# Kernel tuning notes

Hardware: AMD Instinct MI355X
Metric: run time of the kernel (lower is better)

Reference implementation:

```python
import jax, jax.numpy as jnp
import numpy as np

K = 1024   # num_embeddings
E = 64     # embedding_dim
T = 1024   # time
B = 64     # batch
BETA = 0.25  # commitment_cost


def setup_inputs() -> dict:
    key = jax.random.key(0)
    k1, k2 = jax.random.split(key)
    inputs = jax.random.normal(k1, (E, T, B), dtype=jnp.float32)
    # torch init: uniform(-1/num_embeddings, 1/num_embeddings)
    codebook = jax.random.uniform(k2, (K, E), dtype=jnp.float32,
                                  minval=-1.0 / K, maxval=1.0 / K)
    return {"inputs": inputs, "codebook": codebook}


def reference(inputs, codebook):
    # inputs: [E, T, B]; torch does permute(1,2,0) -> [T, B, E]
    x = jnp.transpose(inputs, (1, 2, 0))            # [T, B, E]
    flat = x.reshape(-1, E)                          # [N, E], N = T*B
    d = (jnp.sum(flat * flat, axis=1, keepdims=True)
         + jnp.sum(codebook * codebook, axis=1)
         - 2.0 * (flat @ codebook.T))
    idx = jnp.argmin(d, axis=1)                      # [N]
    # one-hot @ codebook == gather (same math, efficient form)
    q = codebook[idx].reshape(T, B, E)               # [T, B, E]

    e_latent_loss = jnp.mean((jax.lax.stop_gradient(q) - x) ** 2)
    q_latent_loss = jnp.mean((q - jax.lax.stop_gradient(x)) ** 2)
    vq_loss = q_latent_loss + BETA * e_latent_loss

    # straight-through estimator
    q_st = x + jax.lax.stop_gradient(q - x)

    # perplexity from code-usage histogram (mean of one-hots)
    N = flat.shape[0]
    counts = jnp.zeros((K,), jnp.float32).at[idx].add(1.0)
    avg_probs = counts / N
    perplexity = jnp.exp(-jnp.sum(avg_probs * jnp.log(avg_probs + 1e-10)))

    quantized = jnp.transpose(q_st, (2, 0, 1))       # back to [E, T, B]
    return vq_loss, quantized, perplexity
```

## Files before the change

kernel.cpp:

```cpp
#include <hip/hip_runtime.h>


#define KC 1024
#define ED 64
#define NR 65536
#define NE (NR * ED)
#define GAP1 6e-6f

typedef __attribute__((ext_vector_type(8))) short short8;
typedef __attribute__((ext_vector_type(4))) float f32x4;

__device__ __forceinline__ unsigned short bf16rne(float f) {
    unsigned u = __builtin_bit_cast(unsigned, f);
    return (unsigned short)((u + 0x7fffu + ((u >> 16) & 1u)) >> 16);
}
__device__ __forceinline__ float bf16tof(unsigned short h) {
    return __builtin_bit_cast(float, (unsigned)h << 16);
}

__global__ __launch_bounds__(256) void k_pack(const float* __restrict__ cb,
        short8* __restrict__ cbt, unsigned* __restrict__ counts,
        unsigned* __restrict__ flagcnt) {
    const int u = blockIdx.x * 256 + threadIdx.x;
    if (u < 1024) counts[u] = 0u;
    if (u == 1024) *flagcnt = 0u;
    if (u >= 64 * 5 * 64) return;
    const int t = u / 320, rem = u % 320, j = rem / 64, l = rem % 64;
    const int g = l >> 4;
    if (j < 4) {
        const int code = t * 16 + (l & 15);
        const float* c = cb + (size_t)code * ED;
        const bool lo = (j >= 2);
        short8 o;
#pragma unroll
        for (int r = 0; r < 8; ++r) {
            const int e = (j & 1) * 32 + g * 8 + r;
            const float m2 = -2.f * c[e];
            const unsigned short h = bf16rne(m2);
            o[r] = lo ? (short)bf16rne(m2 - bf16tof(h)) : (short)h;
        }
        cbt[u] = o;
    } else {
        f32x4 o;
#pragma unroll
        for (int r = 0; r < 4; ++r) {
            const float4* c4 = (const float4*)(cb + (size_t)(t * 16 + g * 4 + r) * ED);
            float s0 = 0.f, s1 = 0.f, s2 = 0.f, s3 = 0.f;
#pragma unroll
            for (int i = 0; i < 16; ++i) {
                const float4 c = c4[i];
                s0 = fmaf(c.x, c.x, s0); s1 = fmaf(c.y, c.y, s1);
                s2 = fmaf(c.z, c.z, s2); s3 = fmaf(c.w, c.w, s3);
            }
            o[r] = (s0 + s1) + (s2 + s3);
        }
        cbt[u] = __builtin_bit_cast(short8, o);
    }
}

__global__ __launch_bounds__(256) void k_argmin(
        const float* __restrict__ in, const short8* __restrict__ cbt,
        const float* __restrict__ cb, int* __restrict__ idx,
        float* __restrict__ qout, unsigned* __restrict__ counts,
        unsigned* __restrict__ flagcnt, unsigned* __restrict__ flaglist,
        double* __restrict__ pblk) {
    __shared__ short8 xs[8][64];
    __shared__ float rx2p[8][32];
    __shared__ float sb[4][2][16], sb2[4][2][16];
    __shared__ int   sk[4][2][16];
    __shared__ int   fidx[32];

    const int tid = threadIdx.x;
    const int l = tid & 63;
    const int wid = tid >> 6;
    const int g = l >> 4;
    const int col = l & 15;
    const int rowBase = blockIdx.x * 32;

    {
        const int row = tid & 31;
        const int ob = tid >> 5;
        const int hh = ob >> 2, gg = ob & 3;
        const int rt = row >> 4;
        const int ll = gg * 16 + (row & 15);
        float part = 0.f;
        short8 H, L;
#pragma unroll
        for (int j = 0; j < 8; ++j) {
            const float x = in[(size_t)(ob * 8 + j) * NR + rowBase + row];
            const unsigned short hb = bf16rne(x);
            H[j] = (short)hb;
            L[j] = (short)bf16rne(x - bf16tof(hb));
            part = fmaf(x, x, part);
        }
        xs[rt * 4 + hh][ll] = H;
        xs[rt * 4 + 2 + hh][ll] = L;
        rx2p[ob][row] = part;
    }
    __syncthreads();

    const int kh = wid;
    short8 xq[2][4];
#pragma unroll
    for (int rt = 0; rt < 2; ++rt)
#pragma unroll
        for (int q = 0; q < 4; ++q)
            xq[rt][q] = xs[rt * 4 + q][l];

    float best[2]  = {3.4e38f, 3.4e38f};
    float best2[2] = {3.4e38f, 3.4e38f};
    int bestk[2] = {0, 0};

#pragma unroll 2
    for (int tt = 0; tt < 16; ++tt) {
        const int t = kh * 16 + tt;
        const short8* bp = cbt + (size_t)t * 320 + l;
        const short8 b0 = bp[0], b1 = bp[64], b2 = bp[128], b3 = bp[192];
        const f32x4 e4 = __builtin_bit_cast(f32x4, bp[256]);
#pragma unroll
        for (int rt = 0; rt < 2; ++rt) {
            f32x4 acc = e4;
            acc = __builtin_amdgcn_mfma_f32_16x16x32_bf16(b0, xq[rt][0], acc, 0, 0, 0);
            acc = __builtin_amdgcn_mfma_f32_16x16x32_bf16(b1, xq[rt][1], acc, 0, 0, 0);
            acc = __builtin_amdgcn_mfma_f32_16x16x32_bf16(b2, xq[rt][0], acc, 0, 0, 0);
            acc = __builtin_amdgcn_mfma_f32_16x16x32_bf16(b3, xq[rt][1], acc, 0, 0, 0);
            acc = __builtin_amdgcn_mfma_f32_16x16x32_bf16(b0, xq[rt][2], acc, 0, 0, 0);
            acc = __builtin_amdgcn_mfma_f32_16x16x32_bf16(b1, xq[rt][3], acc, 0, 0, 0);
#pragma unroll
            for (int r = 0; r < 4; ++r) {
                const float v = acc[r];
                const int k = t * 16 + g * 4 + r;
                best2[rt] = fminf(fmaxf(v, best[rt]), best2[rt]);
                const bool c = v < best[rt];
                bestk[rt] = c ? k : bestk[rt];
                best[rt]  = fminf(v, best[rt]);
            }
        }
    }

#pragma unroll
    for (int rt = 0; rt < 2; ++rt) {
        float b = best[rt], b2 = best2[rt]; int k = bestk[rt];
#pragma unroll
        for (int sh = 16; sh <= 32; sh <<= 1) {
            const float ob  = __shfl_xor(b, sh, 64);
            const float ob2 = __shfl_xor(b2, sh, 64);
            const int   ok  = __shfl_xor(k, sh, 64);
            if (ob < b || (ob == b && ok < k)) { b2 = fminf(b, ob2); k = ok; b = ob; }
            else b2 = fminf(b2, ob);
        }
        if (g == 0) { sb[wid][rt][col] = b; sb2[wid][rt][col] = b2; sk[wid][rt][col] = k; }
    }
    __syncthreads();

    if (wid == 0) {
        const int rt = (l >> 4) & 1, c2 = l & 15;
        const bool act = (l < 32);
        float b = sb[0][rt][c2], b2 = sb2[0][rt][c2]; int k = sk[0][rt][c2];
#pragma unroll
        for (int s = 1; s < 4; ++s) {
            const float ob = sb[s][rt][c2], ob2 = sb2[s][rt][c2];
            const int ok = sk[s][rt][c2];
            if (ob < b || (ob == b && ok < k)) { b2 = fminf(b, ob2); k = ok; b = ob; }
            else b2 = fminf(b2, ob);
        }
        const int lrow = rt * 16 + c2;
        const int row = rowBase + lrow;
        double d2 = 0.0;
        if (act) {
            idx[row] = k;
            fidx[lrow] = k;
            atomicAdd(&counts[k], 1u);
            if (b2 - b < GAP1) {
                const unsigned p = atomicAdd(flagcnt, 1u);
                flaglist[p] = (unsigned)row;
            }
            float rx = 0.f;
#pragma unroll
            for (int o = 0; o < 8; ++o) rx += rx2p[o][lrow];
            d2 = (double)b + (double)rx;
        }
#pragma unroll
        for (int off = 16; off > 0; off >>= 1) d2 += __shfl_down(d2, off, 64);
        if (l == 0) pblk[blockIdx.x] = d2;
    }
    __syncthreads();

    {
        const int row = tid & 31;
        const int e0 = tid >> 5;
        const int k = fidx[row];
        const float4* c4 = (const float4*)(cb + (size_t)k * ED + e0 * 8);
        const float4 v0 = c4[0], v1 = c4[1];
        qout[(size_t)(e0 * 8 + 0) * NR + rowBase + row] = v0.x;
        qout[(size_t)(e0 * 8 + 1) * NR + rowBase + row] = v0.y;
        qout[(size_t)(e0 * 8 + 2) * NR + rowBase + row] = v0.z;
        qout[(size_t)(e0 * 8 + 3) * NR + rowBase + row] = v0.w;
        qout[(size_t)(e0 * 8 + 4) * NR + rowBase + row] = v1.x;
        qout[(size_t)(e0 * 8 + 5) * NR + rowBase + row] = v1.y;
        qout[(size_t)(e0 * 8 + 6) * NR + rowBase + row] = v1.z;
        qout[(size_t)(e0 * 8 + 7) * NR + rowBase + row] = v1.w;
    }
}

__global__ __launch_bounds__(256) void k_exact64(
        const float* __restrict__ in, const float* __restrict__ cb,
        int* __restrict__ idx, float* __restrict__ qout,
        unsigned* __restrict__ counts,
        const unsigned* __restrict__ flagcnt, const unsigned* __restrict__ flaglist) {
    const unsigned nf = *flagcnt;
    const int l = threadIdx.x & 63;
    const unsigned wave = blockIdx.x * 4u + (unsigned)(threadIdx.x >> 6);
    const unsigned nwave = gridDim.x * 4u;
    for (unsigned i = wave; i < nf; i += nwave) {
        const int row = (int)flaglist[i];
        float x[ED];
#pragma unroll
        for (int e = 0; e < ED; ++e) x[e] = in[(size_t)e * NR + row];
        double best = 1e300; int bestk = 0;
        for (int ci = 0; ci < 16; ++ci) {
            const int k = ci * 64 + l;
            const float* c = cb + (size_t)k * ED;
            double s = 0.0, e2 = 0.0;
            for (int e = 0; e < ED; ++e) {
                const double cv = (double)c[e];
                e2 = fma(cv, cv, e2);
                s  = fma(cv, (double)x[e], s);
            }
            const double t = fma(-2.0, s, e2);
            if (t < best) { best = t; bestk = k; }
        }
        for (int sh = 1; sh < 64; sh <<= 1) {
            const double ob = __shfl_xor(best, sh, 64);
            const int   ok  = __shfl_xor(bestk, sh, 64);
            if (ob < best || (ob == best && ok < bestk)) { best = ob; bestk = ok; }
        }
        const int old = idx[row];
        if (bestk != old) {
            if (l == 0) {
                idx[row] = bestk;
                atomicSub(&counts[old], 1u);
                atomicAdd(&counts[bestk], 1u);
            }
            qout[(size_t)l * NR + row] = cb[(size_t)bestk * ED + l];
        }
    }
}

__global__ __launch_bounds__(1024) void k_final(const unsigned* __restrict__ counts,
        const double* __restrict__ pblk, float* __restrict__ out) {
    __shared__ double redE[16], redS[16];
    const int tid = threadIdx.x;
    const double p = (double)counts[tid] * (1.0 / 65536.0);
    double term = p * log(p + 1e-10);
    double s = pblk[tid] + pblk[tid + 1024];
#pragma unroll
    for (int off = 32; off > 0; off >>= 1) {
        term += __shfl_down(term, off, 64);
        s    += __shfl_down(s,    off, 64);
    }
    if ((tid & 63) == 0) { redE[tid >> 6] = term; redS[tid >> 6] = s; }
    __syncthreads();
    if (tid == 0) {
        double e = 0.0, ss = 0.0;
        for (int i = 0; i < 16; ++i) { e += redE[i]; ss += redS[i]; }
        out[1 + NE] = (float)exp(-e);
        const double m = ss * (1.0 / 4194304.0);
        out[0] = (float)(1.25 * m);
    }
}

extern "C" void kernel_launch(void* const* d_in, const int* in_sizes, int n_in,
                              void* d_out, int out_size, void* d_ws, size_t ws_size,
                              hipStream_t stream) {
    (void)in_sizes; (void)n_in; (void)out_size; (void)ws_size;
    const float* in = (const float*)d_in[0];
    const float* cb = (const float*)d_in[1];
    float* out = (float*)d_out;

    unsigned* counts   = (unsigned*)d_ws;
    unsigned* flagcnt  = (unsigned*)d_ws + 1024;
    short8*   cbt      = (short8*)((float*)d_ws + 2048);
    int*      idx      = (int*)d_ws + 83968;
    unsigned* flaglist = (unsigned*)d_ws + 149504;
    double*   pblk     = (double*)((char*)d_ws + 860160);

    hipLaunchKernelGGL(k_pack,    dim3(80),   dim3(256),  0, stream,
                       cb, cbt, counts, flagcnt);
    hipLaunchKernelGGL(k_argmin,  dim3(2048), dim3(256),  0, stream,
                       in, cbt, cb, idx, out + 1, counts, flagcnt, flaglist, pblk);
    hipLaunchKernelGGL(k_exact64, dim3(256),  dim3(256),  0, stream,
                       in, cb, idx, out + 1, counts, flagcnt, flaglist);
    hipLaunchKernelGGL(k_final,   dim3(1),    dim3(1024), 0, stream,
                       counts, pblk, out);
}
```

Before: 83.75 us.

## Stage codebook tiles in LDS with async double-buffered loads, 128 rows per block

Restructures the argmin kernel so each block handles 128 rows. Each wave owns 32 rows and sweeps all 1024 codes, where before the four waves split the codebook across 32 rows. Codebook tiles are streamed into a double-buffered LDS area with global_load_lds and shared by all waves, which cuts per-wave global codebook traffic and removes the cross-wave reduction through shared memory. In exchange it adds two barriers per tile, shared-memory atomics for row norms, a 4x smaller grid, and a larger workspace layout.

```diff
diff --git a/kernel.cpp b/kernel.cpp
--- a/kernel.cpp
+++ b/kernel.cpp
@@ -17,6 +17,11 @@
 __device__ __forceinline__ float bf16tof(unsigned short h) {
     return __builtin_bit_cast(float, (unsigned)h << 16);
 }
+
+#define GLOAD_LDS16(GSRC, LDST) \
+    __builtin_amdgcn_global_load_lds( \
+        (const __attribute__((address_space(1))) void*)(GSRC), \
+        (__attribute__((address_space(3))) void*)(LDST), 16, 0, 0)
 
 __global__ __launch_bounds__(256) void k_pack(const float* __restrict__ cb,
         short8* __restrict__ cbt, unsigned* __restrict__ counts,
@@ -27,6 +32,7 @@
     if (u >= 64 * 5 * 64) return;
     const int t = u / 320, rem = u % 320, j = rem / 64, l = rem % 64;
     const int g = l >> 4;
+    const int w = t * 512 + (j < 4 ? j * 64 : 256) + l;
     if (j < 4) {
         const int code = t * 16 + (l & 15);
         const float* c = cb + (size_t)code * ED;
@@ -39,7 +45,7 @@
             const unsigned short h = bf16rne(m2);
             o[r] = lo ? (short)bf16rne(m2 - bf16tof(h)) : (short)h;
         }
-        cbt[u] = o;
+        cbt[w] = o;
     } else {
         f32x4 o;
 #pragma unroll
@@ -54,7 +60,7 @@
             }
             o[r] = (s0 + s1) + (s2 + s3);
         }
-        cbt[u] = __builtin_bit_cast(short8, o);
+        cbt[w] = __builtin_bit_cast(short8, o);
     }
 }
 
@@ -64,24 +70,32 @@
         float* __restrict__ qout, unsigned* __restrict__ counts,
         unsigned* __restrict__ flagcnt, unsigned* __restrict__ flaglist,
         double* __restrict__ pblk) {
-    __shared__ short8 xs[8][64];
-    __shared__ float rx2p[8][32];
-    __shared__ float sb[4][2][16], sb2[4][2][16];
-    __shared__ int   sk[4][2][16];
-    __shared__ int   fidx[32];
+    __shared__ short8 xs[4][8][64];
+    __shared__ short8 lbuf[2][512];
+    __shared__ float  rx2s[128];
+    __shared__ int    fidx[128];
 
     const int tid = threadIdx.x;
     const int l = tid & 63;
     const int wid = tid >> 6;
     const int g = l >> 4;
-    const int col = l & 15;
-    const int rowBase = blockIdx.x * 32;
-
-    {
-        const int row = tid & 31;
-        const int ob = tid >> 5;
+    const int rowBase = blockIdx.x * 128;
+
+    if (tid < 128) rx2s[tid] = 0.f;
+    __syncthreads();
+
+    GLOAD_LDS16(cbt + (size_t)0 * 512 + wid * 64 + l, &lbuf[0][wid * 64]);
+    GLOAD_LDS16(cbt + (size_t)0 * 512 + (wid + 4) * 64 + l, &lbuf[0][(wid + 4) * 64]);
+
+#pragma unroll
+    for (int c = 0; c < 4; ++c) {
+        const int task = tid + c * 256;
+        const int row = task & 127;
+        const int ob = task >> 7;
         const int hh = ob >> 2, gg = ob & 3;
-        const int rt = row >> 4;
+        const int w = row >> 5;
+        const int r5 = row & 31;
+        const int rt = r5 >> 4;
         const int ll = gg * 16 + (row & 15);
         float part = 0.f;
         short8 H, L;
@@ -93,30 +107,38 @@
             L[j] = (short)bf16rne(x - bf16tof(hb));
             part = fmaf(x, x, part);
         }
-        xs[rt * 4 + hh][ll] = H;
-        xs[rt * 4 + 2 + hh][ll] = L;
-        rx2p[ob][row] = part;
+        xs[w][rt * 4 + hh][ll] = H;
+        xs[w][rt * 4 + 2 + hh][ll] = L;
+        atomicAdd(&rx2s[row], part);
     }
     __syncthreads();
 
-    const int kh = wid;
     short8 xq[2][4];
 #pragma unroll
     for (int rt = 0; rt < 2; ++rt)
 #pragma unroll
         for (int q = 0; q < 4; ++q)
-            xq[rt][q] = xs[rt * 4 + q][l];
+            xq[rt][q] = xs[wid][rt * 4 + q][l];
 
     float best[2]  = {3.4e38f, 3.4e38f};
     float best2[2] = {3.4e38f, 3.4e38f};
     int bestk[2] = {0, 0};
 
-#pragma unroll 2
-    for (int tt = 0; tt < 16; ++tt) {
-        const int t = kh * 16 + tt;
-        const short8* bp = cbt + (size_t)t * 320 + l;
-        const short8 b0 = bp[0], b1 = bp[64], b2 = bp[128], b3 = bp[192];
-        const f32x4 e4 = __builtin_bit_cast(f32x4, bp[256]);
+    for (int t = 0; t < 64; ++t) {
+        const int cur = t & 1;
+        if (t < 63) {
+            const short8* s_ = cbt + (size_t)(t + 1) * 512;
+            GLOAD_LDS16(s_ + wid * 64 + l, &lbuf[cur ^ 1][wid * 64]);
+            GLOAD_LDS16(s_ + (wid + 4) * 64 + l, &lbuf[cur ^ 1][(wid + 4) * 64]);
+            asm volatile("s_waitcnt vmcnt(2)" ::: "memory");
+        } else {
+            asm volatile("s_waitcnt vmcnt(0)" ::: "memory");
+        }
+        __builtin_amdgcn_s_barrier();
+
+        const short8 b0 = lbuf[cur][0 * 64 + l], b1 = lbuf[cur][1 * 64 + l],
+                     b2 = lbuf[cur][2 * 64 + l], b3 = lbuf[cur][3 * 64 + l];
+        const f32x4 e4 = __builtin_bit_cast(f32x4, lbuf[cur][256 + l]);
 #pragma unroll
         for (int rt = 0; rt < 2; ++rt) {
             f32x4 acc = e4;
@@ -136,8 +158,10 @@
                 best[rt]  = fminf(v, best[rt]);
             }
         }
-    }
-
+        __builtin_amdgcn_s_barrier();
+    }
+
+    double d2 = 0.0;
 #pragma unroll
     for (int rt = 0; rt < 2; ++rt) {
         float b = best[rt], b2 = best2[rt]; int k = bestk[rt];
@@ -149,25 +173,9 @@
             if (ob < b || (ob == b && ok < k)) { b2 = fminf(b, ob2); k = ok; b = ob; }
             else b2 = fminf(b2, ob);
         }
-        if (g == 0) { sb[wid][rt][col] = b; sb2[wid][rt][col] = b2; sk[wid][rt][col] = k; }
-    }
-    __syncthreads();
-
-    if (wid == 0) {
-        const int rt = (l >> 4) & 1, c2 = l & 15;
-        const bool act = (l < 32);
-        float b = sb[0][rt][c2], b2 = sb2[0][rt][c2]; int k = sk[0][rt][c2];
-#pragma unroll
-        for (int s = 1; s < 4; ++s) {
-            const float ob = sb[s][rt][c2], ob2 = sb2[s][rt][c2];
-            const int ok = sk[s][rt][c2];
-            if (ob < b || (ob == b && ok < k)) { b2 = fminf(b, ob2); k = ok; b = ob; }
-            else b2 = fminf(b2, ob);
-        }
-        const int lrow = rt * 16 + c2;
-        const int row = rowBase + lrow;
-        double d2 = 0.0;
-        if (act) {
+        if (l < 16) {
+            const int lrow = wid * 32 + rt * 16 + l;
+            const int row = rowBase + lrow;
             idx[row] = k;
             fidx[lrow] = k;
             atomicAdd(&counts[k], 1u);
@@ -175,31 +183,27 @@
                 const unsigned p = atomicAdd(flagcnt, 1u);
                 flaglist[p] = (unsigned)row;
             }
-            float rx = 0.f;
-#pragma unroll
-            for (int o = 0; o < 8; ++o) rx += rx2p[o][lrow];
-            d2 = (double)b + (double)rx;
-        }
-#pragma unroll
-        for (int off = 16; off > 0; off >>= 1) d2 += __shfl_down(d2, off, 64);
-        if (l == 0) pblk[blockIdx.x] = d2;
-    }
+            d2 += (double)b + (double)rx2s[lrow];
+        }
+    }
+#pragma unroll
+    for (int off = 32; off > 0; off >>= 1) d2 += __shfl_down(d2, off, 64);
+    if (l == 0) pblk[blockIdx.x * 4 + wid] = d2;
     __syncthreads();
 
     {
-        const int row = tid & 31;
-        const int e0 = tid >> 5;
+        const int row = tid & 127;
+        const int e0 = tid >> 7;
         const int k = fidx[row];
-        const float4* c4 = (const float4*)(cb + (size_t)k * ED + e0 * 8);
-        const float4 v0 = c4[0], v1 = c4[1];
-        qout[(size_t)(e0 * 8 + 0) * NR + rowBase + row] = v0.x;
-        qout[(size_t)(e0 * 8 + 1) * NR + rowBase + row] = v0.y;
-        qout[(size_t)(e0 * 8 + 2) * NR + rowBase + row] = v0.z;
-        qout[(size_t)(e0 * 8 + 3) * NR + rowBase + row] = v0.w;
-        qout[(size_t)(e0 * 8 + 4) * NR + rowBase + row] = v1.x;
-        qout[(size_t)(e0 * 8 + 5) * NR + rowBase + row] = v1.y;
-        qout[(size_t)(e0 * 8 + 6) * NR + rowBase + row] = v1.z;
-        qout[(size_t)(e0 * 8 + 7) * NR + rowBase + row] = v1.w;
+        const float4* c4 = (const float4*)(cb + (size_t)k * ED + e0 * 32);
+#pragma unroll
+        for (int j = 0; j < 8; ++j) {
+            const float4 v = c4[j];
+            qout[(size_t)(e0 * 32 + j * 4 + 0) * NR + rowBase + row] = v.x;
+            qout[(size_t)(e0 * 32 + j * 4 + 1) * NR + rowBase + row] = v.y;
+            qout[(size_t)(e0 * 32 + j * 4 + 2) * NR + rowBase + row] = v.z;
+            qout[(size_t)(e0 * 32 + j * 4 + 3) * NR + rowBase + row] = v.w;
+        }
     }
 }
 
@@ -281,16 +285,16 @@
     unsigned* counts   = (unsigned*)d_ws;
     unsigned* flagcnt  = (unsigned*)d_ws + 1024;
     short8*   cbt      = (short8*)((float*)d_ws + 2048);
-    int*      idx      = (int*)d_ws + 83968;
-    unsigned* flaglist = (unsigned*)d_ws + 149504;
-    double*   pblk     = (double*)((char*)d_ws + 860160);
-
-    hipLaunchKernelGGL(k_pack,    dim3(80),   dim3(256),  0, stream,
+    int*      idx      = (int*)d_ws + 133120;
+    unsigned* flaglist = (unsigned*)d_ws + 198656;
+    double*   pblk     = (double*)((char*)d_ws + 1056768);
+
+    hipLaunchKernelGGL(k_pack,    dim3(80),  dim3(256),  0, stream,
                        cb, cbt, counts, flagcnt);
-    hipLaunchKernelGGL(k_argmin,  dim3(2048), dim3(256),  0, stream,
+    hipLaunchKernelGGL(k_argmin,  dim3(512), dim3(256),  0, stream,
                        in, cbt, cb, idx, out + 1, counts, flagcnt, flaglist, pblk);
-    hipLaunchKernelGGL(k_exact64, dim3(256),  dim3(256),  0, stream,
+    hipLaunchKernelGGL(k_exact64, dim3(256), dim3(256),  0, stream,
                        in, cb, idx, out + 1, counts, flagcnt, flaglist);
-    hipLaunchKernelGGL(k_final,   dim3(1),    dim3(1024), 0, stream,
+    hipLaunchKernelGGL(k_final,   dim3(1),   dim3(1024), 0, stream,
                        counts, pblk, out);
 }
```

Result: slower. 109.5 us (+30.7%).
